# Kernel tuning notes

Measured on AMD Instinct MI355X. Metric: run time of the kernel, lower is better.

Reference implementation:

```python
import jax, jax.numpy as jnp
from jax import lax
import numpy as np

B = 32768      # batch
D = 256        # input = hidden = output dim
DEPTH = 9      # universal_depth


def setup_inputs() -> dict:
    key = jax.random.key(0)
    ks = jax.random.split(key, 16)
    s = 1.0 / np.sqrt(D)  # keep pre-activations sane
    r = lambda k, shp, sc=s: (jax.random.normal(k, shp, jnp.float32) * sc)
    return {
        "x": jax.random.normal(ks[0], (B, D), jnp.float32),
        "lin0_w": r(ks[1], (D, D)), "lin0_b": r(ks[2], (D,), 0.1),
        "lin1_w": r(ks[3], (D, D)), "lin1_b": r(ks[4], (D,), 0.1),
        "u1_w": jax.random.normal(ks[5], (DEPTH, D, D), jnp.float32),
        "u1_cw": r(ks[6], (D, D)), "u1_cb": r(ks[7], (D,), 0.1),
        "lin2_w": r(ks[8], (D, D)), "lin2_b": r(ks[9], (D,), 0.1),
        "u2_w": jax.random.normal(ks[10], (DEPTH, D, D), jnp.float32),
        "u2_cw": r(ks[11], (D, D)), "u2_cb": r(ks[12], (D,), 0.1),
        "lino_w": r(ks[13], (D, D)), "lino_b": r(ks[14], (D,), 0.1),
    }


def _universal_layer(x, uw, cw, cb):
    """UniversalNeuralLayer.forward, vectorized.

    The circulant 'gate' matrix implements, for state s of length n:
        s'[i] = cos*s[i] - sin*s[(i+1)%n] + sin*s[(i-1)%n]
    Applied 3 times per depth with angles uw[d, j, 0..2] (j = output unit).
    The result is independent of x and of the batch index.
    """
    n = x.shape[1]
    classical = x @ cw + cb                      # [B, n]
    # angle sequence per output j, in (depth, gate) order -> [3*DEPTH, n]
    angles = jnp.transpose(uw[:, :, :3], (0, 2, 1)).reshape(-1, n)
    init = jnp.full((n, n), 1.0 / np.sqrt(n), dtype=x.dtype)  # [n_j, n_state]

    def step(s, ang):
        c = jnp.cos(ang)[:, None]
        sn = jnp.sin(ang)[:, None]
        return c * s + sn * (jnp.roll(s, 1, axis=1) - jnp.roll(s, -1, axis=1)), None

    s, _ = lax.scan(step, init, angles)
    p = s[:, 0] ** 2                             # |state[0]|^2 per output j
    return jnp.tanh(classical + p[None, :])


def reference(x, lin0_w, lin0_b, lin1_w, lin1_b, u1_w, u1_cw, u1_cb,
              lin2_w, lin2_b, u2_w, u2_cw, u2_cb, lino_w, lino_b):
    h = jax.nn.relu(x @ lin0_w.T + lin0_b)
    h = jax.nn.relu(h @ lin1_w.T + lin1_b)
    h = _universal_layer(h, u1_w, u1_cw, u1_cb)
    h = jax.nn.relu(h @ lin2_w.T + lin2_b)
    h = _universal_layer(h, u2_w, u2_cw, u2_cb)
    return jax.nn.relu(h @ lino_w.T + lino_b)
```

## Files before the change

kernel.cpp:

```cpp
#include <hip/hip_runtime.h>
#include <math.h>

#define DD 256

typedef float  f32x4  __attribute__((ext_vector_type(4)));
typedef short  bf16x8 __attribute__((ext_vector_type(8)));

__device__ __forceinline__ unsigned short f2bf(float f) {
    unsigned int u = __float_as_uint(f);
    u = (u + 0x7fffu + ((u >> 16) & 1u)) >> 16;
    return (unsigned short)u;
}
__device__ __forceinline__ float bf2f(unsigned int h16) {
    return __uint_as_float(h16 << 16);
}

__global__ __launch_bounds__(256)
void prep_all(const float* __restrict__ w0, const float* __restrict__ w1,
              const float* __restrict__ cw1, const float* __restrict__ w2,
              const float* __restrict__ cw2, const float* __restrict__ wo,
              const float* __restrict__ u1_w, const float* __restrict__ u2_w,
              unsigned short* __restrict__ wall, float* __restrict__ p_out) {
    if (blockIdx.x >= 192) {
        const int j = threadIdx.x;
        const int which = blockIdx.x - 192;
        const float* uw = which ? u2_w : u1_w;
        float s = 0.0625f;
#pragma unroll
        for (int d = 0; d < 9; ++d)
#pragma unroll
            for (int g = 0; g < 3; ++g)
                s *= cosf(uw[d * DD * DD + j * DD + g]);
        p_out[which * DD + j] = s * s;
        return;
    }
    const int gid  = blockIdx.x * 256 + threadIdx.x;
    const int mat  = gid >> 13;
    const int rem  = gid & 8191;
    const int wb   = rem >> 11;
    const int rem2 = rem & 2047;
    const int k0   = rem2 >> 8;
    const int rem3 = rem2 & 255;
    const int nt   = rem3 >> 6;
    const int lane = rem3 & 63;
    const int n  = wb * 64 + nt * 16 + (lane & 15);
    const int kb = k0 * 32 + (lane >> 4) * 8;

    const float* src;
    bool tr = false;
    switch (mat) {
        case 0: src = w0; break;
        case 1: src = w1; break;
        case 2: src = cw1; tr = true; break;
        case 3: src = w2; break;
        case 4: src = cw2; tr = true; break;
        default: src = wo; break;
    }
    unsigned short tmp[8];
#pragma unroll
    for (int j = 0; j < 8; ++j) {
        const float v = tr ? src[(kb + j) * DD + n] : src[n * DD + kb + j];
        tmp[j] = f2bf(v);
    }
    *(uint4*)&wall[mat * 65536 + wb * 16384 + k0 * 2048 + nt * 512 + lane * 8] =
        *(const uint4*)tmp;
}

__device__ __forceinline__ int chunk_idx(int m, int kc) {
    return kc * 32 + (m ^ (kc & 7));
}

__device__ __forceinline__ float fast_tanh(float x) {
    const float e = __expf(2.0f * x);
    return 1.0f - 2.0f * __builtin_amdgcn_rcpf(1.0f + e);
}

__device__ __forceinline__ void lds_barrier() {
    asm volatile("s_waitcnt lgkmcnt(0)" ::: "memory");
    __builtin_amdgcn_s_barrier();
}

template <int MODE>
__device__ __forceinline__ void layer_step(const uint4* hr, uint4* hw,
                                           bf16x8 (&wr)[2][4],
                                           const unsigned short* __restrict__ Wb,
                                           const unsigned short* __restrict__ Wnb,
                                           const float* __restrict__ bias,
                                           const float* __restrict__ pv,
                                           float* __restrict__ out, int m0) {
    const int tid  = threadIdx.x;
    const int wave = tid >> 6;
    const int lane = tid & 63;
    const int quad = lane >> 4;
    const int l15  = lane & 15;

    f32x4 acc[4][2];
#pragma unroll
    for (int nt = 0; nt < 4; ++nt)
#pragma unroll
        for (int mt = 0; mt < 2; ++mt) acc[nt][mt] = (f32x4){0.f, 0.f, 0.f, 0.f};

    bf16x8 h_f[2][2];
#pragma unroll
    for (int mt = 0; mt < 2; ++mt)
        h_f[0][mt] = *(const bf16x8*)&hr[chunk_idx(mt * 16 + l15, quad)];

#pragma unroll
    for (int k0 = 0; k0 < 8; ++k0) {
        const int cur = k0 & 1, nxt = cur ^ 1;
        {
            const unsigned short* ws = (k0 < 7) ? &Wb[(k0 + 1) * 2048] : Wnb;
#pragma unroll
            for (int nt = 0; nt < 4; ++nt)
                wr[nxt][nt] = *(const bf16x8*)&ws[nt * 512];
        }
        if (k0 < 7) {
            const int kc = (k0 + 1) * 4 + quad;
#pragma unroll
            for (int mt = 0; mt < 2; ++mt)
                h_f[nxt][mt] = *(const bf16x8*)&hr[chunk_idx(mt * 16 + l15, kc)];
        }
#pragma unroll
        for (int nt = 0; nt < 4; ++nt)
#pragma unroll
            for (int mt = 0; mt < 2; ++mt)
                acc[nt][mt] = __builtin_amdgcn_mfma_f32_16x16x32_bf16(
                    wr[cur][nt], h_f[cur][mt], acc[nt][mt], 0, 0, 0);
    }

    const int nb = wave * 64;
    f32x4 addv[4];
#pragma unroll
    for (int nt = 0; nt < 4; ++nt) {
        const int n0 = nb + nt * 16 + quad * 4;
        addv[nt] = *(const f32x4*)&bias[n0];
        if (MODE == 1) addv[nt] += *(const f32x4*)&pv[n0];
    }

#pragma unroll
    for (int nt = 0; nt < 4; ++nt) {
        const int n0   = nb + nt * 16 + quad * 4;
        const int kc_o = n0 >> 3;
        const int half = quad & 1;
#pragma unroll
        for (int mt = 0; mt < 2; ++mt) {
            const f32x4 v = acc[nt][mt] + addv[nt];
            if (MODE == 2) {
                f32x4 r;
                r.x = fmaxf(v.x, 0.f); r.y = fmaxf(v.y, 0.f);
                r.z = fmaxf(v.z, 0.f); r.w = fmaxf(v.w, 0.f);
                *(f32x4*)&out[(size_t)(m0 + mt * 16 + l15) * DD + n0] = r;
            } else {
                float t0, t1, t2, t3;
                if (MODE == 1) {
                    t0 = fast_tanh(v.x); t1 = fast_tanh(v.y);
                    t2 = fast_tanh(v.z); t3 = fast_tanh(v.w);
                } else {
                    t0 = fmaxf(v.x, 0.f); t1 = fmaxf(v.y, 0.f);
                    t2 = fmaxf(v.z, 0.f); t3 = fmaxf(v.w, 0.f);
                }
                uint2 u;
                u.x = (unsigned int)f2bf(t0) | ((unsigned int)f2bf(t1) << 16);
                u.y = (unsigned int)f2bf(t2) | ((unsigned int)f2bf(t3) << 16);
                *(uint2*)((char*)&hw[chunk_idx(mt * 16 + l15, kc_o)] + half * 8) = u;
            }
        }
    }
    if (MODE != 2) lds_barrier();
}

__global__ __launch_bounds__(256, 4)
void unet_fused(const float* __restrict__ x,
                const unsigned short* __restrict__ wall,
                const float* __restrict__ b0, const float* __restrict__ b1,
                const float* __restrict__ cb1, const float* __restrict__ b2,
                const float* __restrict__ cb2, const float* __restrict__ bo,
                const float* __restrict__ pbuf,
                float* __restrict__ out) {
    __shared__ uint4 hbuf[2048];
    uint4* hA = hbuf;
    uint4* hB = hbuf + 1024;
    const int m0   = blockIdx.x * 32;
    const int tid  = threadIdx.x;
    const int wave = tid >> 6;
    const int lane = tid & 63;

    const unsigned short* WB = wall + wave * 16384 + lane * 8;

    bf16x8 wr[2][4];
#pragma unroll
    for (int nt = 0; nt < 4; ++nt)
        wr[0][nt] = *(const bf16x8*)&WB[nt * 512];

    const int c4     = tid & 63;
    const int rbase  = wave * 8;
    const int kc_s   = c4 >> 1;
    const int half_s = c4 & 1;
#pragma unroll
    for (int i = 0; i < 8; ++i) {
        const int row = rbase + i;
        const float4 v = *(const float4*)&x[(size_t)(m0 + row) * DD + c4 * 4];
        uint2 u;
        u.x = (unsigned int)f2bf(v.x) | ((unsigned int)f2bf(v.y) << 16);
        u.y = (unsigned int)f2bf(v.z) | ((unsigned int)f2bf(v.w) << 16);
        *(uint2*)((char*)&hA[chunk_idx(row, kc_s)] + half_s * 8) = u;
    }
    lds_barrier();

    layer_step<0>(hA, hB, wr, WB + 0 * 65536, WB + 1 * 65536, b0, nullptr,
                  nullptr, 0);
    layer_step<0>(hB, hA, wr, WB + 1 * 65536, WB + 2 * 65536, b1, nullptr,
                  nullptr, 0);
    layer_step<1>(hA, hB, wr, WB + 2 * 65536, WB + 3 * 65536, cb1, pbuf,
                  nullptr, 0);
    layer_step<0>(hB, hA, wr, WB + 3 * 65536, WB + 4 * 65536, b2, nullptr,
                  nullptr, 0);
    layer_step<1>(hA, hB, wr, WB + 4 * 65536, WB + 5 * 65536, cb2, pbuf + 256,
                  nullptr, 0);
    layer_step<2>(hB, nullptr, wr, WB + 5 * 65536, WB + 0 * 65536, bo, nullptr,
                  out, m0);
}

extern "C" void kernel_launch(void* const* d_in, const int* in_sizes, int n_in,
                              void* d_out, int out_size, void* d_ws, size_t ws_size,
                              hipStream_t stream) {
    const float* x      = (const float*)d_in[0];
    const float* lin0_w = (const float*)d_in[1];
    const float* lin0_b = (const float*)d_in[2];
    const float* lin1_w = (const float*)d_in[3];
    const float* lin1_b = (const float*)d_in[4];
    const float* u1_w   = (const float*)d_in[5];
    const float* u1_cw  = (const float*)d_in[6];
    const float* u1_cb  = (const float*)d_in[7];
    const float* lin2_w = (const float*)d_in[8];
    const float* lin2_b = (const float*)d_in[9];
    const float* u2_w   = (const float*)d_in[10];
    const float* u2_cw  = (const float*)d_in[11];
    const float* u2_cb  = (const float*)d_in[12];
    const float* lino_w = (const float*)d_in[13];
    const float* lino_b = (const float*)d_in[14];

    float* out = (float*)d_out;
    unsigned short* wall = (unsigned short*)d_ws;
    float* pbuf = (float*)((char*)d_ws + 6 * 65536 * 2);

    prep_all<<<dim3(194), dim3(256), 0, stream>>>(
        lin0_w, lin1_w, u1_cw, lin2_w, u2_cw, lino_w, u1_w, u2_w, wall, pbuf);
    unet_fused<<<dim3(1024), dim3(256), 0, stream>>>(
        x, wall, lin0_b, lin1_b, u1_cb, lin2_b, u2_cb, lino_b, pbuf, out);
}
```

Baseline: 158.0 us.

## Deepen weight prefetch to three stages and use single in-place LDS buffer

```diff
diff --git a/kernel.cpp b/kernel.cpp
--- a/kernel.cpp
+++ b/kernel.cpp
@@ -75,14 +75,8 @@
     return 1.0f - 2.0f * __builtin_amdgcn_rcpf(1.0f + e);
 }
 
-__device__ __forceinline__ void lds_barrier() {
-    asm volatile("s_waitcnt lgkmcnt(0)" ::: "memory");
-    __builtin_amdgcn_s_barrier();
-}
-
 template <int MODE>
-__device__ __forceinline__ void layer_step(const uint4* hr, uint4* hw,
-                                           bf16x8 (&wr)[2][4],
+__device__ __forceinline__ void layer_step(uint4* h, bf16x8 (&wr)[4][4],
                                            const unsigned short* __restrict__ Wb,
                                            const unsigned short* __restrict__ Wnb,
                                            const float* __restrict__ bias,
@@ -103,29 +97,29 @@
     bf16x8 h_f[2][2];
 #pragma unroll
     for (int mt = 0; mt < 2; ++mt)
-        h_f[0][mt] = *(const bf16x8*)&hr[chunk_idx(mt * 16 + l15, quad)];
+        h_f[0][mt] = *(const bf16x8*)&h[chunk_idx(mt * 16 + l15, quad)];
 
 #pragma unroll
     for (int k0 = 0; k0 < 8; ++k0) {
-        const int cur = k0 & 1, nxt = cur ^ 1;
         {
-            const unsigned short* ws = (k0 < 7) ? &Wb[(k0 + 1) * 2048] : Wnb;
+            const int t = k0 + 3;
+            const unsigned short* ws = (t < 8) ? &Wb[t * 2048] : &Wnb[(t - 8) * 2048];
 #pragma unroll
             for (int nt = 0; nt < 4; ++nt)
-                wr[nxt][nt] = *(const bf16x8*)&ws[nt * 512];
+                wr[t & 3][nt] = *(const bf16x8*)&ws[nt * 512];
         }
         if (k0 < 7) {
             const int kc = (k0 + 1) * 4 + quad;
 #pragma unroll
             for (int mt = 0; mt < 2; ++mt)
-                h_f[nxt][mt] = *(const bf16x8*)&hr[chunk_idx(mt * 16 + l15, kc)];
+                h_f[(k0 + 1) & 1][mt] = *(const bf16x8*)&h[chunk_idx(mt * 16 + l15, kc)];
         }
 #pragma unroll
         for (int nt = 0; nt < 4; ++nt)
 #pragma unroll
             for (int mt = 0; mt < 2; ++mt)
                 acc[nt][mt] = __builtin_amdgcn_mfma_f32_16x16x32_bf16(
-                    wr[cur][nt], h_f[cur][mt], acc[nt][mt], 0, 0, 0);
+                    wr[k0 & 3][nt], h_f[k0 & 1][mt], acc[nt][mt], 0, 0, 0);
     }
 
     const int nb = wave * 64;
@@ -136,6 +130,8 @@
         addv[nt] = *(const f32x4*)&bias[n0];
         if (MODE == 1) addv[nt] += *(const f32x4*)&pv[n0];
     }
+
+    if (MODE != 2) __syncthreads();
 
 #pragma unroll
     for (int nt = 0; nt < 4; ++nt) {
@@ -162,11 +158,11 @@
                 uint2 u;
                 u.x = (unsigned int)f2bf(t0) | ((unsigned int)f2bf(t1) << 16);
                 u.y = (unsigned int)f2bf(t2) | ((unsigned int)f2bf(t3) << 16);
-                *(uint2*)((char*)&hw[chunk_idx(mt * 16 + l15, kc_o)] + half * 8) = u;
+                *(uint2*)((char*)&h[chunk_idx(mt * 16 + l15, kc_o)] + half * 8) = u;
             }
         }
     }
-    if (MODE != 2) lds_barrier();
+    if (MODE != 2) __syncthreads();
 }
 
 __global__ __launch_bounds__(256, 4)
@@ -177,9 +173,7 @@
                 const float* __restrict__ cb2, const float* __restrict__ bo,
                 const float* __restrict__ pbuf,
                 float* __restrict__ out) {
-    __shared__ uint4 hbuf[2048];
-    uint4* hA = hbuf;
-    uint4* hB = hbuf + 1024;
+    __shared__ uint4 h[1024];
     const int m0   = blockIdx.x * 32;
     const int tid  = threadIdx.x;
     const int wave = tid >> 6;
@@ -187,10 +181,12 @@
 
     const unsigned short* WB = wall + wave * 16384 + lane * 8;
 
-    bf16x8 wr[2][4];
-#pragma unroll
-    for (int nt = 0; nt < 4; ++nt)
-        wr[0][nt] = *(const bf16x8*)&WB[nt * 512];
+    bf16x8 wr[4][4];
+#pragma unroll
+    for (int t = 0; t < 3; ++t)
+#pragma unroll
+        for (int nt = 0; nt < 4; ++nt)
+            wr[t][nt] = *(const bf16x8*)&WB[t * 2048 + nt * 512];
 
     const int c4     = tid & 63;
     const int rbase  = wave * 8;
@@ -203,21 +199,21 @@
         uint2 u;
         u.x = (unsigned int)f2bf(v.x) | ((unsigned int)f2bf(v.y) << 16);
         u.y = (unsigned int)f2bf(v.z) | ((unsigned int)f2bf(v.w) << 16);
-        *(uint2*)((char*)&hA[chunk_idx(row, kc_s)] + half_s * 8) = u;
-    }
-    lds_barrier();
-
-    layer_step<0>(hA, hB, wr, WB + 0 * 65536, WB + 1 * 65536, b0, nullptr,
-                  nullptr, 0);
-    layer_step<0>(hB, hA, wr, WB + 1 * 65536, WB + 2 * 65536, b1, nullptr,
-                  nullptr, 0);
-    layer_step<1>(hA, hB, wr, WB + 2 * 65536, WB + 3 * 65536, cb1, pbuf,
-                  nullptr, 0);
-    layer_step<0>(hB, hA, wr, WB + 3 * 65536, WB + 4 * 65536, b2, nullptr,
-                  nullptr, 0);
-    layer_step<1>(hA, hB, wr, WB + 4 * 65536, WB + 5 * 65536, cb2, pbuf + 256,
-                  nullptr, 0);
-    layer_step<2>(hB, nullptr, wr, WB + 5 * 65536, WB + 0 * 65536, bo, nullptr,
+        *(uint2*)((char*)&h[chunk_idx(row, kc_s)] + half_s * 8) = u;
+    }
+    __syncthreads();
+
+    layer_step<0>(h, wr, WB + 0 * 65536, WB + 1 * 65536, b0, nullptr,
+                  nullptr, 0);
+    layer_step<0>(h, wr, WB + 1 * 65536, WB + 2 * 65536, b1, nullptr,
+                  nullptr, 0);
+    layer_step<1>(h, wr, WB + 2 * 65536, WB + 3 * 65536, cb1, pbuf,
+                  nullptr, 0);
+    layer_step<0>(h, wr, WB + 3 * 65536, WB + 4 * 65536, b2, nullptr,
+                  nullptr, 0);
+    layer_step<1>(h, wr, WB + 4 * 65536, WB + 5 * 65536, cb2, pbuf + 256,
+                  nullptr, 0);
+    layer_step<2>(h, wr, WB + 5 * 65536, WB + 0 * 65536, bo, nullptr,
                   out, m0);
 }
 
```

After: 149.8 us. -5.2%, faster.
